# Kernel tuning notes

Hardware: AMD Instinct MI355X
Metric: run time of the kernel (lower is better)

The kernel has to match this reference:

```python
import jax, jax.numpy as jnp
import numpy as np
import math

D_MODEL = 1024
NHEAD = 16
D_K = D_MODEL // NHEAD
LAMDA_ATT = 1.0
B, L = 2, 2048


def setup_inputs() -> dict:
    key = jax.random.key(0)
    ks = jax.random.split(key, 10)
    s = 1.0 / math.sqrt(D_MODEL)
    x = jax.random.normal(ks[0], (B, L, D_MODEL), dtype=jnp.float32)
    delta_r = jax.random.uniform(ks[1], (B, L), dtype=jnp.float32)  # positive, fed to log
    Wq = jax.random.normal(ks[2], (D_MODEL, D_MODEL), dtype=jnp.float32) * s
    Wk = jax.random.normal(ks[3], (D_MODEL, D_MODEL), dtype=jnp.float32) * s
    Wv = jax.random.normal(ks[4], (D_MODEL, D_MODEL), dtype=jnp.float32) * s
    Wo = jax.random.normal(ks[5], (D_MODEL, D_MODEL), dtype=jnp.float32) * s
    bq = jnp.zeros((D_MODEL,), jnp.float32)
    bk = jnp.zeros((D_MODEL,), jnp.float32)
    bv = jnp.zeros((D_MODEL,), jnp.float32)
    bo = jnp.zeros((D_MODEL,), jnp.float32)
    return {"x": x, "delta_r": delta_r, "Wq": Wq, "bq": bq, "Wk": Wk, "bk": bk,
            "Wv": Wv, "bv": bv, "Wo": Wo, "bo": bo}


def reference(x, delta_r, Wq, bq, Wk, bk, Wv, bv, Wo, bo):
    b, l, d = x.shape
    h, dk = NHEAD, D_K

    def proj(y, W, bias):
        # [B,L,D] -> [B,H,L,dk]
        return (y @ W + bias).reshape(b, l, h, dk).transpose(0, 2, 1, 3)

    v_scaled = x * delta_r[..., None]
    q = proj(x, Wq, bq)
    k = proj(x, Wk, bk)
    v = proj(v_scaled, Wv, bv)

    scores = jnp.einsum('bhqd,bhkd->bhqk', q, k) / math.sqrt(dk)
    pos = jnp.arange(l)
    dist = jnp.abs(pos[None, :] - pos[:, None]).astype(scores.dtype)  # [L,L]
    rel_bias = LAMDA_ATT * jnp.log(delta_r + 1e-6)  # [B,L]
    scores = scores - dist[None, None] * 0.1 + rel_bias[:, None, None, :]

    attn = jax.nn.softmax(scores, axis=-1)  # dropout is identity in eval mode
    context = jnp.einsum('bhqk,bhkd->bqhd', attn, v).reshape(b, l, d)
    out = context @ Wo + bo
    return out, attn.mean(axis=1)
```

## Files before the change

kernel.cpp:

```cpp
#include <hip/hip_runtime.h>
#include <math.h>

#define DMODEL 1024
#define NHEAD  16
#define DK     64
#define BB     2
#define LL     2048
#define MTOT   (BB*LL)

#define LOG2E      1.4426950408889634f
#define SCQ        (0.125f * LOG2E)
#define C2LOG      (0.1f * LOG2E)
#define SKIP_BOUND (-24.0f)

typedef __bf16 bf16_t;
typedef __bf16 bf16x8 __attribute__((ext_vector_type(8)));
typedef __bf16 bf16x4 __attribute__((ext_vector_type(4)));
typedef float  f32x4  __attribute__((ext_vector_type(4)));

static __device__ __forceinline__ f32x4 mfma16(bf16x8 a, bf16x8 b, f32x4 c) {
    return __builtin_amdgcn_mfma_f32_16x16x32_bf16(a, b, c, 0, 0, 0);
}
static __device__ __forceinline__ float exp2f_fast(float x) {
    return __builtin_amdgcn_exp2f(x);
}
static __device__ __forceinline__ float log2f_fast(float x) {
    return __builtin_amdgcn_logf(x);
}
static __device__ __forceinline__ void gl_lds16(const bf16_t* g, bf16_t* l) {
    __builtin_amdgcn_global_load_lds(
        (const __attribute__((address_space(1))) unsigned int*)g,
        (__attribute__((address_space(3))) unsigned int*)l, 16, 0, 0);
}

__global__ __launch_bounds__(256) void prep_fused_k(
    const float* __restrict__ x, const float* __restrict__ dr,
    bf16_t* __restrict__ xb, float* __restrict__ logd2,
    const float* __restrict__ Wq, const float* __restrict__ Wk,
    const float* __restrict__ Wv, const float* __restrict__ Wo,
    bf16_t* __restrict__ Wcat, bf16_t* __restrict__ Wot)
{
    __shared__ __align__(16) float Ts[64][68];
    const int bid = blockIdx.x;
    const int tid = threadIdx.x;
    if (bid < 2048) {
        size_t gid = (size_t)bid * 256 + tid;
        size_t off = gid * 8;
        float4 a = *(const float4*)(x + off);
        float4 c = *(const float4*)(x + off + 4);
        float va[8] = {a.x, a.y, a.z, a.w, c.x, c.y, c.z, c.w};
        bf16x8 o1;
#pragma unroll
        for (int j = 0; j < 8; ++j) o1[j] = (bf16_t)va[j];
        *(bf16x8*)(xb + off) = o1;
        if (gid < MTOT) logd2[gid] = log2f_fast(dr[gid] + 1e-6f);
    } else {
        const int t = bid - 2048;
        const int z = t >> 8;
        const float* W = (z == 0) ? Wq : (z == 1) ? Wk : (z == 2) ? Wv : Wo;
        bf16_t* dst = (z < 3) ? (Wcat + (size_t)z * DMODEL * DMODEL) : Wot;
        const int k0 = (t & 15) * 64, n0 = ((t >> 4) & 15) * 64;
#pragma unroll
        for (int i = 0; i < 4; ++i) {
            int u = tid + 256 * i, r = u >> 4, c4 = (u & 15) * 4;
            *(float4*)&Ts[r][c4] = *(const float4*)(W + (size_t)(k0 + r) * DMODEL + n0 + c4);
        }
        __syncthreads();
#pragma unroll
        for (int i = 0; i < 2; ++i) {
            int u = tid + 256 * i, n = u >> 3, k8 = (u & 7) * 8;
            bf16x8 v;
#pragma unroll
            for (int j = 0; j < 8; ++j) v[j] = (bf16_t)Ts[k8 + j][n];
            *(bf16x8*)(dst + (size_t)(n0 + n) * DMODEL + k0 + k8) = v;
        }
    }
}

__global__ __launch_bounds__(256, 3) void gemm128_k(
    const bf16_t* __restrict__ A, const bf16_t* __restrict__ Bt,
    const float* __restrict__ b0, const float* __restrict__ b1,
    const float* __restrict__ b2, const float* __restrict__ delta,
    bf16_t* __restrict__ outQ, bf16_t* __restrict__ outK,
    bf16_t* __restrict__ outVt)
{
    __shared__ __align__(16) bf16_t Asw[128 * 64];
    __shared__ __align__(16) bf16_t Bsw[128 * 64];
    const int tid = threadIdx.x, lane = tid & 63, w = tid >> 6;
    const int quad = lane >> 4, n16 = lane & 15;
    const int wm = (w & 1) * 64, wn = (w >> 1) * 64;
    const int m0 = blockIdx.y * 128, n0 = blockIdx.x * 128;
    const int srow = lane >> 3;
    const int scb  = (lane & 7) ^ srow;

    f32x4 acc[4][4] = {};

    for (int K0 = 0; K0 < DMODEL; K0 += 64) {
        __syncthreads();
#pragma unroll
        for (int i = 0; i < 4; ++i) {
            int rb = w * 32 + i * 8;
            gl_lds16(A  + (size_t)(m0 + rb + srow) * DMODEL + K0 + scb * 8,
                     &Asw[rb * 64]);
            gl_lds16(Bt + (size_t)(n0 + rb + srow) * DMODEL + K0 + scb * 8,
                     &Bsw[rb * 64]);
        }
        __syncthreads();
#pragma unroll
        for (int kc = 0; kc < 2; ++kc) {
            const int pcb = ((kc * 4 + quad) ^ (n16 & 7)) * 8;
            bf16x8 af[4], bfv[4];
#pragma unroll
            for (int mi = 0; mi < 4; ++mi)
                af[mi] = *(const bf16x8*)&Asw[(wm + mi * 16 + n16) * 64 + pcb];
#pragma unroll
            for (int ni = 0; ni < 4; ++ni)
                bfv[ni] = *(const bf16x8*)&Bsw[(wn + ni * 16 + n16) * 64 + pcb];
#pragma unroll
            for (int mi = 0; mi < 4; ++mi)
#pragma unroll
                for (int ni = 0; ni < 4; ++ni)
                    acc[mi][ni] = mfma16(af[mi], bfv[ni], acc[mi][ni]);
        }
    }

    const int region = n0 >> 10;
    if (region == 2) {
#pragma unroll
        for (int mi = 0; mi < 4; ++mi) {
            const int mbase = m0 + wm + mi * 16 + quad * 4;
            const int bidx = mbase >> 11, l = mbase & (LL - 1);
            const f32x4 dm4 = *(const f32x4*)(delta + mbase);
#pragma unroll
            for (int ni = 0; ni < 4; ++ni) {
                const int nl = (n0 & 1023) + wn + ni * 16 + n16;
                const int h = nl >> 6, dd = nl & 63;
                const float bv = b2[nl];
                bf16x4 pk;
#pragma unroll
                for (int r = 0; r < 4; ++r)
                    pk[r] = (bf16_t)(acc[mi][ni][r] * dm4[r] + bv);
                *(bf16x4*)(outVt + ((size_t)(bidx * NHEAD + h) * DK + dd) * LL + l) = pk;
            }
        }
    } else {
        const float* bias = (region == 0) ? b0 : b1;
        bf16_t* dst = (region == 0) ? outQ : outK;
        const float qs = (region == 0) ? SCQ : 1.0f;
#pragma unroll
        for (int mi = 0; mi < 4; ++mi) {
#pragma unroll
            for (int r = 0; r < 4; ++r) {
                const int m = m0 + wm + mi * 16 + quad * 4 + r;
                const int bidx = m >> 11, l = m & (LL - 1);
#pragma unroll
                for (int ni = 0; ni < 4; ++ni) {
                    const int nl = (n0 & 1023) + wn + ni * 16 + n16;
                    const int h = nl >> 6, dd = nl & 63;
                    float v = (acc[mi][ni][r] + bias[nl]) * qs;
                    dst[(((size_t)(bidx * NHEAD + h) * LL) + l) * DK + dd] = (bf16_t)v;
                }
            }
        }
    }
}

__global__ __launch_bounds__(256) void stats_k(
    const bf16_t* __restrict__ Q, const bf16_t* __restrict__ K,
    const float* __restrict__ logd2, float* __restrict__ Qn,
    float* __restrict__ Kn, float* __restrict__ dlb, float* __restrict__ ldx)
{
    __shared__ float qn_s[256], kn_s[256], dg_s[256];
    const int blk = blockIdx.x;
    const int bh = blk >> 3, seg = blk & 7, b = bh >> 4;
    const int tid = threadIdx.x;
    const int row = seg * 256 + tid;
    const size_t base = (size_t)bh * LL * DK;

    float qn2 = 0.f, kn2 = 0.f, dg = 0.f;
#pragma unroll
    for (int j = 0; j < 8; ++j) {
        bf16x8 qv = *(const bf16x8*)(Q + base + (size_t)row * DK + j * 8);
        bf16x8 kv = *(const bf16x8*)(K + base + (size_t)row * DK + j * 8);
#pragma unroll
        for (int e = 0; e < 8; ++e) {
            float fq = (float)qv[e], fk = (float)kv[e];
            qn2 += fq * fq; kn2 += fk * fk; dg += fq * fk;
        }
    }
    qn_s[tid] = qn2;
    kn_s[tid] = kn2;
    dg_s[tid] = dg + logd2[b * LL + row];
    __syncthreads();

    if (tid < 2) {
        float mq = 0.f, md = 1e30f;
        for (int r = 0; r < 128; ++r) {
            mq = fmaxf(mq, qn_s[tid * 128 + r]);
            md = fminf(md, dg_s[tid * 128 + r]);
        }
        Qn[bh * 16 + seg * 2 + tid] = sqrtf(mq);
        dlb[bh * 16 + seg * 2 + tid] = md;
    } else if (tid >= 64 && tid < 68) {
        const int t = tid - 64;
        float mk = 0.f;
        for (int r = 0; r < 64; ++r) mk = fmaxf(mk, kn_s[t * 64 + r]);
        Kn[bh * 32 + seg * 4 + t] = sqrtf(mk);
    } else if (tid >= 128 && tid < 132 && (bh & 15) == 0) {
        const int t = tid - 128;
        float ml = -1e30f;
        for (int r = 0; r < 64; ++r)
            ml = fmaxf(ml, logd2[b * LL + seg * 256 + t * 64 + r]);
        ldx[b * 32 + seg * 4 + t] = ml;
    }
}

__global__ __launch_bounds__(256, 4) void attn_flash_mfma_k(
    const bf16_t* __restrict__ Q, const bf16_t* __restrict__ K,
    const bf16_t* __restrict__ Vt, const float* __restrict__ logd2,
    const float* __restrict__ Qn, const float* __restrict__ Kn,
    const float* __restrict__ dlb, const float* __restrict__ ldx,
    bf16_t* __restrict__ ctx, float* __restrict__ mlout,
    float* __restrict__ mlmin64)
{
    __shared__ __align__(16) bf16_t Ks[64][72];
    __shared__ __align__(16) bf16_t Vts[64][72];
    __shared__ __align__(16) bf16_t Ps[4][16][72];
    __shared__ float logds[64];
    __shared__ float wvmin[4];

    const int tid = threadIdx.x;
    const int lane = tid & 63, w = tid >> 6;
    const int quad = lane >> 4, n16 = lane & 15;
    const int bh = blockIdx.x, b = bh >> 4, h = bh & 15;
    const int qt = blockIdx.y, q0 = qt * 64;
    const size_t base = (size_t)bh * LL * DK;
    const int q = q0 + w * 16 + n16;

    bf16x8 qa[2];
#pragma unroll
    for (int kc = 0; kc < 2; ++kc)
        qa[kc] = *(const bf16x8*)(Q + base + (size_t)q * DK + kc * 32 + quad * 8);

    unsigned mask = 0;
    {
        const float qn = Qn[bh * 16 + (qt >> 1)], dl = dlb[bh * 16 + (qt >> 1)];
        for (int t = 0; t < 32; ++t) {
            const int kc0 = t * 64;
            const int dmin = (kc0 > q0 + 63) ? (kc0 - (q0 + 63))
                           : ((q0 > kc0 + 63) ? (q0 - (kc0 + 63)) : 0);
            const float bound = qn * Kn[bh * 32 + t] + ldx[b * 32 + t]
                              - C2LOG * (float)dmin - dl;
            if (bound > SKIP_BOUND) mask |= (1u << t);
        }
    }

    const int strow = tid >> 3, stc8 = (tid & 7) * 8;
    bf16x8 kr0, kr1, vr0, vr1;
    float ldr = 0.f;
    auto prefetch = [&](int k0) {
        kr0 = *(const bf16x8*)(K + base + (size_t)(k0 + strow) * DK + stc8);
        kr1 = *(const bf16x8*)(K + base + (size_t)(k0 + 32 + strow) * DK + stc8);
        vr0 = *(const bf16x8*)(Vt + base + (size_t)strow * LL + k0 + stc8);
        vr1 = *(const bf16x8*)(Vt + base + (size_t)(32 + strow) * LL + k0 + stc8);
        if (tid < 64) ldr = logd2[b * LL + k0 + tid];
    };

    float m_c = -1e30f, l_c = 0.f;
    f32x4 o[4] = {};
    const float dfq = (float)(q - quad * 4);

    int t = (int)__builtin_ctz(mask);
    prefetch(t * 64);
    for (;;) {
        const unsigned rem = (t < 31) ? (mask >> (t + 1)) : 0u;
        const int tn = rem ? (t + 1 + (int)__builtin_ctz(rem)) : -1;
        __syncthreads();
        *(bf16x8*)&Ks[strow][stc8]       = kr0;
        *(bf16x8*)&Ks[32 + strow][stc8]  = kr1;
        *(bf16x8*)&Vts[strow][stc8]      = vr0;
        *(bf16x8*)&Vts[32 + strow][stc8] = vr1;
        if (tid < 64) logds[tid] = ldr;
        __syncthreads();
        if (tn >= 0) prefetch(tn * 64);
        const int k0 = t * 64;

        f32x4 s[4] = {};
#pragma unroll
        for (int kc = 0; kc < 2; ++kc) {
#pragma unroll
            for (int kt = 0; kt < 4; ++kt) {
                bf16x8 kb = *(const bf16x8*)&Ks[kt * 16 + n16][kc * 32 + quad * 8];
                s[kt] = mfma16(kb, qa[kc], s[kt]);
            }
        }
        const float df = dfq - (float)k0;
#pragma unroll
        for (int kt = 0; kt < 4; ++kt) {
            f32x4 ldv = *(const f32x4*)&logds[kt * 16 + quad * 4];
#pragma unroll
            for (int r = 0; r < 4; ++r)
                s[kt][r] += ldv[r] - C2LOG * fabsf(df - (float)(kt * 16 + r));
        }
        f32x4 mx;
#pragma unroll
        for (int r = 0; r < 4; ++r)
            mx[r] = fmaxf(fmaxf(s[0][r], s[1][r]), fmaxf(s[2][r], s[3][r]));
        float rm = fmaxf(fmaxf(mx[0], mx[1]), fmaxf(mx[2], mx[3]));
        rm = fmaxf(rm, __shfl_xor(rm, 16));
        rm = fmaxf(rm, __shfl_xor(rm, 32));
        const float mn = fmaxf(m_c, rm);
        const float alpha = exp2f_fast(m_c - mn);
        if (__any(mn > m_c)) {
#pragma unroll
            for (int dt = 0; dt < 4; ++dt)
#pragma unroll
                for (int r = 0; r < 4; ++r) o[dt][r] *= alpha;
        }
        f32x4 ps = {0.f, 0.f, 0.f, 0.f};
#pragma unroll
        for (int kt = 0; kt < 4; ++kt)
#pragma unroll
            for (int r = 0; r < 4; ++r) {
                float p = exp2f_fast(s[kt][r] - mn);
                s[kt][r] = p;
                ps[r] += p;
            }
        float psum = (ps[0] + ps[1]) + (ps[2] + ps[3]);
        psum += __shfl_xor(psum, 16);
        psum += __shfl_xor(psum, 32);
        l_c = l_c * alpha + psum;
        m_c = mn;
#pragma unroll
        for (int kt = 0; kt < 4; ++kt) {
            bf16x4 pk;
#pragma unroll
            for (int r = 0; r < 4; ++r) pk[r] = (bf16_t)s[kt][r];
            *(bf16x4*)&Ps[w][n16][kt * 16 + quad * 4] = pk;
        }
        __threadfence_block();
#pragma unroll
        for (int kc = 0; kc < 2; ++kc) {
            bf16x8 pa = *(const bf16x8*)&Ps[w][n16][kc * 32 + quad * 8];
#pragma unroll
            for (int dt = 0; dt < 4; ++dt) {
                bf16x8 vb = *(const bf16x8*)&Vts[dt * 16 + n16][kc * 32 + quad * 8];
                o[dt] = mfma16(vb, pa, o[dt]);
            }
        }
        if (tn < 0) break;
        t = tn;
    }
    const float inv = 1.f / l_c;
#pragma unroll
    for (int dt = 0; dt < 4; ++dt) {
        bf16x4 ov;
#pragma unroll
        for (int r = 0; r < 4; ++r) ov[r] = (bf16_t)(o[dt][r] * inv);
        *(bf16x4*)(ctx + ((size_t)b * LL + q) * DMODEL + h * DK +
                   dt * 16 + quad * 4) = ov;
    }
    float mlv = m_c + log2f_fast(l_c);
    if (quad == 0)
        mlout[(size_t)bh * LL + q] = mlv;
    mlv = fminf(mlv, __shfl_xor(mlv, 1));
    mlv = fminf(mlv, __shfl_xor(mlv, 2));
    mlv = fminf(mlv, __shfl_xor(mlv, 4));
    mlv = fminf(mlv, __shfl_xor(mlv, 8));
    if (lane == 0) wvmin[w] = mlv;
    __syncthreads();
    if (tid == 0)
        mlmin64[bh * 32 + qt] = fminf(fminf(wvmin[0], wvmin[1]),
                                      fminf(wvmin[2], wvmin[3]));
}

__global__ __launch_bounds__(256, 3) void tail_fused_k(
    const bf16_t* __restrict__ A, const bf16_t* __restrict__ Bt,
    const float* __restrict__ b0, float* __restrict__ outf,
    const bf16_t* __restrict__ Q, const bf16_t* __restrict__ K,
    const float* __restrict__ logd2, const float* __restrict__ mlws,
    const float* __restrict__ Qn, const float* __restrict__ Kn,
    const float* __restrict__ ml64, const float* __restrict__ ldx,
    float* __restrict__ outmean)
{
    __shared__ __align__(16) char smem[24576];

    const int bid = blockIdx.x;
    const int tid = threadIdx.x;
    const int lane = tid & 63, w = tid >> 6;
    const int quad = lane >> 4, n16 = lane & 15;

    if (bid < 512) {
        bf16_t* Asw = (bf16_t*)smem;
        bf16_t* Bsw = (bf16_t*)(smem + 8192);
        const int wm = (w & 1) * 32, wn = (w >> 1) * 64;
        const int m0 = (bid >> 3) * 64, n0 = (bid & 7) * 128;
        const int srow = lane >> 3;
        const int scb  = (lane & 7) ^ srow;

        f32x4 acc[2][4] = {};

        for (int K0 = 0; K0 < DMODEL; K0 += 64) {
            __syncthreads();
#pragma unroll
            for (int i = 0; i < 2; ++i) {
                int rb = w * 16 + i * 8;
                gl_lds16(A + (size_t)(m0 + rb + srow) * DMODEL + K0 + scb * 8,
                         &Asw[rb * 64]);
            }
#pragma unroll
            for (int i = 0; i < 4; ++i) {
                int rb = w * 32 + i * 8;
                gl_lds16(Bt + (size_t)(n0 + rb + srow) * DMODEL + K0 + scb * 8,
                         &Bsw[rb * 64]);
            }
            __syncthreads();
#pragma unroll
            for (int kc = 0; kc < 2; ++kc) {
                const int pcb = ((kc * 4 + quad) ^ (n16 & 7)) * 8;
                bf16x8 af[2], bfv[4];
#pragma unroll
                for (int mi = 0; mi < 2; ++mi)
                    af[mi] = *(const bf16x8*)&Asw[(wm + mi * 16 + n16) * 64 + pcb];
#pragma unroll
                for (int ni = 0; ni < 4; ++ni)
                    bfv[ni] = *(const bf16x8*)&Bsw[(wn + ni * 16 + n16) * 64 + pcb];
#pragma unroll
                for (int mi = 0; mi < 2; ++mi)
#pragma unroll
                    for (int ni = 0; ni < 4; ++ni)
                        acc[mi][ni] = mfma16(af[mi], bfv[ni], acc[mi][ni]);
            }
        }
#pragma unroll
        for (int mi = 0; mi < 2; ++mi) {
#pragma unroll
            for (int r = 0; r < 4; ++r) {
                const int m = m0 + wm + mi * 16 + quad * 4 + r;
#pragma unroll
                for (int ni = 0; ni < 4; ++ni) {
                    const int n = n0 + wn + ni * 16 + n16;
                    outf[(size_t)m * DMODEL + n] = acc[mi][ni][r] + b0[n];
                }
            }
        }
        return;
    }

    typedef bf16_t KsRow[64][72];
    KsRow* Ks = (KsRow*)smem;
    float (*mls)[128] = (float(*)[128])(smem + 18432);
    float* logds = (float*)(smem + 19456);

    const int tb = bid - 512;
    const int k0 = (tb & 31) * 64, q0 = ((tb >> 5) & 15) * 128, b = tb >> 9;
    const int qq[2] = {q0 + w * 32 + n16, q0 + w * 32 + 16 + n16};

    if (tid < 64) logds[tid] = logd2[b * LL + k0 + tid];
    __syncthreads();

    float bias0[2][4][4];
#pragma unroll
    for (int qg = 0; qg < 2; ++qg) {
        const float df = (float)(qq[qg] - k0 - quad * 4);
#pragma unroll
        for (int kt = 0; kt < 4; ++kt) {
            f32x4 ldv = *(const f32x4*)&logds[kt * 16 + quad * 4];
#pragma unroll
            for (int r = 0; r < 4; ++r)
                bias0[qg][kt][r] = ldv[r] - C2LOG * fabsf(df - (float)(kt * 16 + r));
        }
    }

    const int ktl = k0 >> 6, qt64 = q0 >> 6;
    const int dmin = (k0 > q0 + 127) ? (k0 - (q0 + 127))
                   : ((q0 > k0 + 63) ? (q0 - (k0 + 63)) : 0);
    unsigned hmask = 0;
    {
        const float dterm = ldx[b * 32 + ktl] - C2LOG * (float)dmin;
        const int qt = q0 >> 7;
        for (int h = 0; h < NHEAD; ++h) {
            const int bh = b * 16 + h;
            const float mlmin128 = fminf(ml64[bh * 32 + qt64],
                                         ml64[bh * 32 + qt64 + 1]);
            const float bound = Qn[bh * 16 + qt] * Kn[bh * 32 + ktl] + dterm
                              - mlmin128;
            if (bound > SKIP_BOUND) hmask |= (1u << h);
        }
    }

    f32x4 acc[2][4] = {};

    if (hmask) {
        const int strow = tid >> 3, stc8 = (tid & 7) * 8;
        bf16x8 kr0, kr1, qan[2][2];
        float mlv = 0.f;
        auto load_head = [&](int h) {
            const size_t hb = (size_t)(b * NHEAD + h) * LL * DK;
            kr0 = *(const bf16x8*)(K + hb + (size_t)(k0 + strow) * DK + stc8);
            kr1 = *(const bf16x8*)(K + hb + (size_t)(k0 + 32 + strow) * DK + stc8);
#pragma unroll
            for (int qg = 0; qg < 2; ++qg)
#pragma unroll
                for (int kc = 0; kc < 2; ++kc)
                    qan[qg][kc] = *(const bf16x8*)(Q + hb + (size_t)qq[qg] * DK +
                                                   kc * 32 + quad * 8);
            if (tid < 128) mlv = mlws[(size_t)(b * NHEAD + h) * LL + q0 + tid];
        };

        int h = (int)__builtin_ctz(hmask);
        load_head(h);
        int pc = 0;
        for (;;) {
            const unsigned rem = (h < 15) ? (hmask >> (h + 1)) : 0u;
            const int hn = rem ? (h + 1 + (int)__builtin_ctz(rem)) : -1;
            const int p = pc & 1;
            *(bf16x8*)&Ks[p][strow][stc8]      = kr0;
            *(bf16x8*)&Ks[p][32 + strow][stc8] = kr1;
            if (tid < 128) mls[p][tid] = mlv;
            bf16x8 qc[2][2] = {{qan[0][0], qan[0][1]}, {qan[1][0], qan[1][1]}};
            __syncthreads();
            if (hn >= 0) load_head(hn);

            f32x4 s[2][4] = {};
#pragma unroll
            for (int kc = 0; kc < 2; ++kc) {
#pragma unroll
                for (int kt = 0; kt < 4; ++kt) {
                    bf16x8 kb = *(const bf16x8*)&Ks[p][kt * 16 + n16][kc * 32 + quad * 8];
                    s[0][kt] = mfma16(kb, qc[0][kc], s[0][kt]);
                    s[1][kt] = mfma16(kb, qc[1][kc], s[1][kt]);
                }
            }
#pragma unroll
            for (int qg = 0; qg < 2; ++qg) {
                const float ml = mls[p][w * 32 + qg * 16 + n16];
#pragma unroll
                for (int kt = 0; kt < 4; ++kt)
#pragma unroll
                    for (int r = 0; r < 4; ++r)
                        acc[qg][kt][r] += exp2f_fast(s[qg][kt][r] +
                                                     bias0[qg][kt][r] - ml);
            }
            ++pc;
            if (hn < 0) break;
            h = hn;
        }
    }

    const float invH = 1.f / (float)NHEAD;
#pragma unroll
    for (int qg = 0; qg < 2; ++qg)
#pragma unroll
        for (int kt = 0; kt < 4; ++kt) {
            f32x4 ov;
#pragma unroll
            for (int r = 0; r < 4; ++r) ov[r] = acc[qg][kt][r] * invH;
            *(f32x4*)(outmean + ((size_t)b * LL + qq[qg]) * LL + k0 +
                      kt * 16 + quad * 4) = ov;
        }
}

extern "C" void kernel_launch(void* const* d_in, const int* in_sizes, int n_in,
                              void* d_out, int out_size, void* d_ws, size_t ws_size,
                              hipStream_t stream) {
    const float* x  = (const float*)d_in[0];
    const float* dr = (const float*)d_in[1];
    const float* Wq = (const float*)d_in[2];
    const float* bq = (const float*)d_in[3];
    const float* Wk = (const float*)d_in[4];
    const float* bk = (const float*)d_in[5];
    const float* Wv = (const float*)d_in[6];
    const float* bv = (const float*)d_in[7];
    const float* Wo = (const float*)d_in[8];
    const float* bo = (const float*)d_in[9];
    float* out = (float*)d_out;
    char* ws = (char*)d_ws;
    const size_t MB = 1ull << 20;

    bf16_t* xb   = (bf16_t*)(ws);
    bf16_t* Wcat = (bf16_t*)(ws + 8 * MB);
    bf16_t* Wot  = (bf16_t*)(ws + 14 * MB);
    bf16_t* Qb   = (bf16_t*)(ws + 16 * MB);
    bf16_t* Kb   = (bf16_t*)(ws + 24 * MB);
    bf16_t* Vtb  = (bf16_t*)(ws + 32 * MB);
    float*  logd = (float*)(ws + 40 * MB);
    float*  mlws = (float*)(ws + 41 * MB);
    float*  Qns  = (float*)(ws + 42 * MB);
    float*  Kns  = (float*)(ws + 42 * MB + 4096);
    float*  dlb  = (float*)(ws + 42 * MB + 12288);
    float*  ldxp = (float*)(ws + 42 * MB + 16384);
    float*  ml64 = (float*)(ws + 42 * MB + 20480);
    bf16_t* ctx  = xb;

    prep_fused_k<<<3072, 256, 0, stream>>>(x, dr, xb, logd,
                                           Wq, Wk, Wv, Wo, Wcat, Wot);

    gemm128_k<<<dim3(24, 32), 256, 0, stream>>>(xb, Wcat, bq, bk, bv, dr,
                                                Qb, Kb, Vtb);
    stats_k<<<256, 256, 0, stream>>>(Qb, Kb, logd, Qns, Kns, dlb, ldxp);

    attn_flash_mfma_k<<<dim3(32, 32), 256, 0, stream>>>(Qb, Kb, Vtb, logd,
                                                        Qns, Kns, dlb, ldxp,
                                                        ctx, mlws, ml64);
    tail_fused_k<<<1536, 256, 0, stream>>>(ctx, Wot, bo, out,
                                           Qb, Kb, logd, mlws, Qns, Kns,
                                           ml64, ldxp,
                                           out + (size_t)MTOT * DMODEL);
}
```

Baseline: 213.9 us.

## Reorder attention-mean tiles by diagonal distance and shrink tiles to 64x64

The attention-mean part of the fused tail kernel now uses 64x64 query-key tiles instead of 128x64. Blocks are ranked so that tiles nearest the diagonal (most heads active) launch first, and the output-projection GEMM blocks are moved to the end of the grid. Fully skipped tiles write zeros and return early, before any LDS setup. The smaller tiles give a tighter per-tile skip bound and better load balance, at the cost of more blocks and less K reuse per block.

```diff
diff --git a/kernel.cpp b/kernel.cpp
--- a/kernel.cpp
+++ b/kernel.cpp
@@ -390,11 +390,12 @@
     const int lane = tid & 63, w = tid >> 6;
     const int quad = lane >> 4, n16 = lane & 15;
 
-    if (bid < 512) {
+    if (bid >= 2048) {
         bf16_t* Asw = (bf16_t*)smem;
         bf16_t* Bsw = (bf16_t*)(smem + 8192);
+        const int gb = bid - 2048;
         const int wm = (w & 1) * 32, wn = (w >> 1) * 64;
-        const int m0 = (bid >> 3) * 64, n0 = (bid & 7) * 128;
+        const int m0 = (gb >> 3) * 64, n0 = (gb & 7) * 128;
         const int srow = lane >> 3;
         const int scb  = (lane & 7) ^ srow;
 
@@ -447,65 +448,89 @@
         return;
     }
 
-    typedef bf16_t KsRow[64][72];
-    KsRow* Ks = (KsRow*)smem;
-    float (*mls)[128] = (float(*)[128])(smem + 18432);
-    float* logds = (float*)(smem + 19456);
-
-    const int tb = bid - 512;
-    const int k0 = (tb & 31) * 64, q0 = ((tb >> 5) & 15) * 128, b = tb >> 9;
-    const int qq[2] = {q0 + w * 32 + n16, q0 + w * 32 + 16 + n16};
-
-    if (tid < 64) logds[tid] = logd2[b * LL + k0 + tid];
-    __syncthreads();
-
-    float bias0[2][4][4];
-#pragma unroll
-    for (int qg = 0; qg < 2; ++qg) {
-        const float df = (float)(qq[qg] - k0 - quad * 4);
-#pragma unroll
-        for (int kt = 0; kt < 4; ++kt) {
-            f32x4 ldv = *(const f32x4*)&logds[kt * 16 + quad * 4];
-#pragma unroll
-            for (int r = 0; r < 4; ++r)
-                bias0[qg][kt][r] = ldv[r] - C2LOG * fabsf(df - (float)(kt * 16 + r));
-        }
-    }
-
-    const int ktl = k0 >> 6, qt64 = q0 >> 6;
-    const int dmin = (k0 > q0 + 127) ? (k0 - (q0 + 127))
+    const int rank = bid >> 6, bq = bid & 63, b = bq >> 5, q64i = bq & 31;
+    const int q0 = q64i * 64;
+
+    int ktile = 0;
+    {
+        const int c = q64i;
+        int want = rank;
+        for (int d = 0; d < 32; ++d) {
+            int ka = c - d;
+            if (ka >= 0) {
+                if (want == 0) { ktile = ka; break; }
+                --want;
+            }
+            int kb2 = c + d;
+            if (d > 0 && kb2 < 32) {
+                if (want == 0) { ktile = kb2; break; }
+                --want;
+            }
+        }
+    }
+    const int k0 = ktile * 64;
+
+    const int qt = q0 >> 7;
+    const int qt64 = q0 >> 6;
+    const int dmin = (k0 > q0 + 63) ? (k0 - (q0 + 63))
                    : ((q0 > k0 + 63) ? (q0 - (k0 + 63)) : 0);
     unsigned hmask = 0;
     {
-        const float dterm = ldx[b * 32 + ktl] - C2LOG * (float)dmin;
-        const int qt = q0 >> 7;
+        const float dterm = ldx[b * 32 + ktile] - C2LOG * (float)dmin;
         for (int h = 0; h < NHEAD; ++h) {
             const int bh = b * 16 + h;
-            const float mlmin128 = fminf(ml64[bh * 32 + qt64],
-                                         ml64[bh * 32 + qt64 + 1]);
-            const float bound = Qn[bh * 16 + qt] * Kn[bh * 32 + ktl] + dterm
-                              - mlmin128;
+            const float bound = Qn[bh * 16 + qt] * Kn[bh * 32 + ktile] + dterm
+                              - ml64[bh * 32 + qt64];
             if (bound > SKIP_BOUND) hmask |= (1u << h);
         }
     }
 
-    f32x4 acc[2][4] = {};
-
-    if (hmask) {
+    if (!hmask) {
+        const int row = tid >> 2, c4 = (tid & 3) * 4;
+        const f32x4 z = {0.f, 0.f, 0.f, 0.f};
+        float* dst = outmean + ((size_t)b * LL + q0 + row) * LL + k0 + c4;
+#pragma unroll
+        for (int cc = 0; cc < 4; ++cc)
+            *(f32x4*)(dst + cc * 16) = z;
+        return;
+    }
+
+    typedef bf16_t KsRow[64][72];
+    KsRow* Ks = (KsRow*)smem;
+    float (*mls)[64] = (float(*)[64])(smem + 18432);
+    float* logds = (float*)(smem + 18944);
+
+    const int qq = q0 + w * 16 + n16;
+
+    if (tid < 64) logds[tid] = logd2[b * LL + k0 + tid];
+    __syncthreads();
+
+    float bias0[4][4];
+    {
+        const float df = (float)(qq - k0 - quad * 4);
+#pragma unroll
+        for (int kt = 0; kt < 4; ++kt) {
+            f32x4 ldv = *(const f32x4*)&logds[kt * 16 + quad * 4];
+#pragma unroll
+            for (int r = 0; r < 4; ++r)
+                bias0[kt][r] = ldv[r] - C2LOG * fabsf(df - (float)(kt * 16 + r));
+        }
+    }
+
+    f32x4 acc[4] = {};
+    {
         const int strow = tid >> 3, stc8 = (tid & 7) * 8;
-        bf16x8 kr0, kr1, qan[2][2];
+        bf16x8 kr0, kr1, qan[2];
         float mlv = 0.f;
         auto load_head = [&](int h) {
             const size_t hb = (size_t)(b * NHEAD + h) * LL * DK;
             kr0 = *(const bf16x8*)(K + hb + (size_t)(k0 + strow) * DK + stc8);
             kr1 = *(const bf16x8*)(K + hb + (size_t)(k0 + 32 + strow) * DK + stc8);
 #pragma unroll
-            for (int qg = 0; qg < 2; ++qg)
-#pragma unroll
-                for (int kc = 0; kc < 2; ++kc)
-                    qan[qg][kc] = *(const bf16x8*)(Q + hb + (size_t)qq[qg] * DK +
-                                                   kc * 32 + quad * 8);
-            if (tid < 128) mlv = mlws[(size_t)(b * NHEAD + h) * LL + q0 + tid];
+            for (int kc = 0; kc < 2; ++kc)
+                qan[kc] = *(const bf16x8*)(Q + hb + (size_t)qq * DK +
+                                           kc * 32 + quad * 8);
+            if (tid < 64) mlv = mlws[(size_t)(b * NHEAD + h) * LL + q0 + tid];
         };
 
         int h = (int)__builtin_ctz(hmask);
@@ -517,31 +542,26 @@
             const int p = pc & 1;
             *(bf16x8*)&Ks[p][strow][stc8]      = kr0;
             *(bf16x8*)&Ks[p][32 + strow][stc8] = kr1;
-            if (tid < 128) mls[p][tid] = mlv;
-            bf16x8 qc[2][2] = {{qan[0][0], qan[0][1]}, {qan[1][0], qan[1][1]}};
+            if (tid < 64) mls[p][tid] = mlv;
+            bf16x8 qc[2] = {qan[0], qan[1]};
             __syncthreads();
             if (hn >= 0) load_head(hn);
 
-            f32x4 s[2][4] = {};
+            f32x4 s[4] = {};
 #pragma unroll
             for (int kc = 0; kc < 2; ++kc) {
 #pragma unroll
                 for (int kt = 0; kt < 4; ++kt) {
                     bf16x8 kb = *(const bf16x8*)&Ks[p][kt * 16 + n16][kc * 32 + quad * 8];
-                    s[0][kt] = mfma16(kb, qc[0][kc], s[0][kt]);
-                    s[1][kt] = mfma16(kb, qc[1][kc], s[1][kt]);
+                    s[kt] = mfma16(kb, qc[kc], s[kt]);
                 }
             }
-#pragma unroll
-            for (int qg = 0; qg < 2; ++qg) {
-                const float ml = mls[p][w * 32 + qg * 16 + n16];
-#pragma unroll
-                for (int kt = 0; kt < 4; ++kt)
-#pragma unroll
-                    for (int r = 0; r < 4; ++r)
-                        acc[qg][kt][r] += exp2f_fast(s[qg][kt][r] +
-                                                     bias0[qg][kt][r] - ml);
-            }
+            const float ml = mls[p][w * 16 + n16];
+#pragma unroll
+            for (int kt = 0; kt < 4; ++kt)
+#pragma unroll
+                for (int r = 0; r < 4; ++r)
+                    acc[kt][r] += exp2f_fast(s[kt][r] + bias0[kt][r] - ml);
             ++pc;
             if (hn < 0) break;
             h = hn;
@@ -550,15 +570,13 @@
 
     const float invH = 1.f / (float)NHEAD;
 #pragma unroll
-    for (int qg = 0; qg < 2; ++qg)
-#pragma unroll
-        for (int kt = 0; kt < 4; ++kt) {
-            f32x4 ov;
-#pragma unroll
-            for (int r = 0; r < 4; ++r) ov[r] = acc[qg][kt][r] * invH;
-            *(f32x4*)(outmean + ((size_t)b * LL + qq[qg]) * LL + k0 +
-                      kt * 16 + quad * 4) = ov;
-        }
+    for (int kt = 0; kt < 4; ++kt) {
+        f32x4 ov;
+#pragma unroll
+        for (int r = 0; r < 4; ++r) ov[r] = acc[kt][r] * invH;
+        *(f32x4*)(outmean + ((size_t)b * LL + qq) * LL + k0 +
+                  kt * 16 + quad * 4) = ov;
+    }
 }
 
 extern "C" void kernel_launch(void* const* d_in, const int* in_sizes, int n_in,
@@ -603,7 +621,7 @@
     attn_flash_mfma_k<<<dim3(32, 32), 256, 0, stream>>>(Qb, Kb, Vtb, logd,
                                                         Qns, Kns, dlb, ldxp,
                                                         ctx, mlws, ml64);
-    tail_fused_k<<<1536, 256, 0, stream>>>(ctx, Wot, bo, out,
+    tail_fused_k<<<2560, 256, 0, stream>>>(ctx, Wot, bo, out,
                                            Qb, Kb, logd, mlws, Qns, Kns,
                                            ml64, ldxp,
                                            out + (size_t)MTOT * DMODEL);
```

After: 208.8 us. -2.4%, faster.
